# Optimization experiments

Measured on AMD Instinct MI355X. Metric: run time of the kernel, lower is better.

Reference implementation:

```python
import jax, jax.numpy as jnp
import numpy as np
import math

D_MODEL = 1024
NUM_HEADS = 16
HEAD_DIM = D_MODEL // NUM_HEADS  # 64


def setup_inputs() -> dict:
    key = jax.random.key(0)
    ks = jax.random.split(key, 5)
    B, T = 4, 2048
    scale = 1.0 / math.sqrt(D_MODEL)
    return {
        "x": jax.random.normal(ks[0], (B, T, D_MODEL), dtype=jnp.float32),
        "wq": jax.random.normal(ks[1], (D_MODEL, D_MODEL), dtype=jnp.float32) * scale,
        "wk": jax.random.normal(ks[2], (D_MODEL, D_MODEL), dtype=jnp.float32) * scale,
        "wv": jax.random.normal(ks[3], (D_MODEL, D_MODEL), dtype=jnp.float32) * scale,
        "wo": jax.random.normal(ks[4], (D_MODEL, D_MODEL), dtype=jnp.float32) * scale,
    }


def reference(x, wq, wk, wv, wo):
    B, T, _ = x.shape
    H, Dk = NUM_HEADS, HEAD_DIM

    def split_heads(t):  # [B,T,D] -> [B,H,T,Dk]
        return t.reshape(B, T, H, Dk).transpose(0, 2, 1, 3)

    q = split_heads(x @ wq)
    k = split_heads(x @ wk)
    v = split_heads(x @ wv)

    # scaled QK^T: [B,H,T,T]
    scores = jnp.einsum("bhqd,bhkd->bhqk", q, k) / jnp.sqrt(jnp.float32(Dk))
    # causal mask: triu(ones, diag=0).T.bool() == lower-triangular incl. diagonal
    causal = jnp.tril(jnp.ones((T, T), dtype=bool))
    scores = jnp.where(causal, scores, -jnp.inf)
    attn = jax.nn.softmax(scores, axis=-1)

    out = jnp.einsum("bhqk,bhkd->bhqd", attn, v)  # [B,H,T,Dk]
    out = out.transpose(0, 2, 1, 3).reshape(B, T, H * Dk)
    return out @ wo
```

## Files before the change

kernel.cpp:

```cpp
#include <hip/hip_runtime.h>
#include <hip/hip_bf16.h>
#include <stdint.h>

typedef __attribute__((ext_vector_type(8))) short bf16x8;
typedef __attribute__((ext_vector_type(4))) float f32x4;
typedef __attribute__((ext_vector_type(4))) unsigned short u16x4;
typedef __attribute__((ext_vector_type(4))) float float4v;

#define MFMA16(a, b, c) __builtin_amdgcn_mfma_f32_16x16x32_bf16((a), (b), (c), 0, 0, 0)

__device__ __forceinline__ unsigned short f2bf(float f) {
  return __builtin_bit_cast(unsigned short, (__bf16)f);
}

typedef const __attribute__((address_space(1))) void* gptr1_t;
typedef __attribute__((address_space(3))) void* lptr3_t;
__device__ __forceinline__ void gload16(const void* g, void* l) {
  __builtin_amdgcn_global_load_lds((gptr1_t)g, (lptr3_t)l, 16, 0, 0);
}

__global__ __launch_bounds__(256) void cvt_x_kernel(const float* __restrict__ in,
                                                    unsigned short* __restrict__ out) {
  int i = blockIdx.x * 256 + threadIdx.x;
  float4v f = ((const float4v*)in)[i];
  u16x4 o;
  o[0] = f2bf(f[0]); o[1] = f2bf(f[1]); o[2] = f2bf(f[2]); o[3] = f2bf(f[3]);
  ((u16x4*)out)[i] = o;
}

__global__ __launch_bounds__(256) void wt_cvt_kernel(const float* __restrict__ w0,
                                                     const float* __restrict__ w1,
                                                     const float* __restrict__ w2,
                                                     const float* __restrict__ w3,
                                                     unsigned short* __restrict__ out) {
  const float* in = blockIdx.z == 0 ? w0 : blockIdx.z == 1 ? w1 : blockIdx.z == 2 ? w2 : w3;
  unsigned short* o = out + (size_t)blockIdx.z * 1024 * 1024;
  __shared__ float tile[32][33];
  int tx = threadIdx.x & 31, ty = threadIdx.x >> 5;
  int c0 = blockIdx.x * 32, r0 = blockIdx.y * 32;
#pragma unroll
  for (int i = 0; i < 4; i++)
    tile[ty + 8 * i][tx] = in[(size_t)(r0 + ty + 8 * i) * 1024 + c0 + tx];
  __syncthreads();
#pragma unroll
  for (int i = 0; i < 4; i++)
    o[(size_t)(c0 + ty + 8 * i) * 1024 + r0 + tx] = f2bf(tile[tx][ty + 8 * i]);
}

template <bool OUTF32>
__global__ __launch_bounds__(256) void gemm128_kernel(
    const unsigned short* __restrict__ A,
    const unsigned short* __restrict__ B0, const unsigned short* __restrict__ B1,
    const unsigned short* __restrict__ B2,
    void* C0, void* C1, void* C2) {
  constexpr int K = 1024, N = 1024;
  const unsigned short* Bt = blockIdx.z == 0 ? B0 : blockIdx.z == 1 ? B1 : B2;
  void* Cv = blockIdx.z == 0 ? C0 : blockIdx.z == 1 ? C1 : C2;

  __shared__ unsigned short As[128 * 32];
  __shared__ unsigned short Bs[128 * 32];

  const int tid = threadIdx.x;
  const int w = tid >> 6, lane = tid & 63, l15 = lane & 15, l4 = lane >> 4;
  const int wm = w >> 1, wn = w & 1;
  const int m0 = blockIdx.x * 128, n0 = blockIdx.y * 128;

  f32x4 acc[4][4] = {};

  const int srow = w * 32 + (lane >> 2);
  const int scol = (lane & 3) * 8;
  const unsigned short* ga = A + (size_t)(m0 + srow) * K + scol;
  const unsigned short* gb = Bt + (size_t)(n0 + srow) * K + scol;
  char* lA = (char*)As + w * 2048;
  char* lB = (char*)Bs + w * 2048;

  for (int k0 = 0; k0 < K; k0 += 32) {
    __syncthreads();
    gload16(ga + k0, lA);
    gload16(ga + k0 + 16 * K, lA + 1024);
    gload16(gb + k0, lB);
    gload16(gb + k0 + 16 * K, lB + 1024);
    __syncthreads();

    bf16x8 af[4], bfr[4];
#pragma unroll
    for (int mi = 0; mi < 4; mi++)
      af[mi] = *(const bf16x8*)&As[(wm * 64 + mi * 16 + l15) * 32 + 8 * l4];
#pragma unroll
    for (int ni = 0; ni < 4; ni++)
      bfr[ni] = *(const bf16x8*)&Bs[(wn * 64 + ni * 16 + l15) * 32 + 8 * l4];
#pragma unroll
    for (int mi = 0; mi < 4; mi++)
#pragma unroll
      for (int ni = 0; ni < 4; ni++)
        acc[mi][ni] = MFMA16(af[mi], bfr[ni], acc[mi][ni]);
  }

#pragma unroll
  for (int mi = 0; mi < 4; mi++)
#pragma unroll
    for (int ni = 0; ni < 4; ni++)
#pragma unroll
      for (int r = 0; r < 4; r++) {
        int mg = m0 + wm * 64 + mi * 16 + 4 * l4 + r;
        int ng = n0 + wn * 64 + ni * 16 + l15;
        if (OUTF32)
          ((float*)Cv)[(size_t)mg * N + ng] = acc[mi][ni][r];
        else
          ((unsigned short*)Cv)[(size_t)mg * N + ng] = f2bf(acc[mi][ni][r]);
      }
}

__global__ __launch_bounds__(256) void gemm64_kernel(const unsigned short* __restrict__ A,
                                                     const unsigned short* __restrict__ Bt,
                                                     float* __restrict__ Cv) {
  constexpr int K = 1024, N = 1024;
  __shared__ unsigned short As[64 * 32];
  __shared__ unsigned short Bs[128 * 32];

  const int tid = threadIdx.x;
  const int w = tid >> 6, lane = tid & 63, l15 = lane & 15, l4 = lane >> 4;
  const int wm = w >> 1, wn = w & 1;
  const int m0 = blockIdx.x * 64, n0 = blockIdx.y * 128;

  f32x4 acc[2][4] = {};

  const int arow = w * 16 + (lane >> 2);
  const int brow = w * 32 + (lane >> 2);
  const int scol = (lane & 3) * 8;
  const unsigned short* ga = A + (size_t)(m0 + arow) * K + scol;
  const unsigned short* gb = Bt + (size_t)(n0 + brow) * K + scol;
  char* lA = (char*)As + w * 1024;
  char* lB = (char*)Bs + w * 2048;

  for (int k0 = 0; k0 < K; k0 += 32) {
    __syncthreads();
    gload16(ga + k0, lA);
    gload16(gb + k0, lB);
    gload16(gb + k0 + 16 * K, lB + 1024);
    __syncthreads();

    bf16x8 af[2], bfr[4];
#pragma unroll
    for (int mi = 0; mi < 2; mi++)
      af[mi] = *(const bf16x8*)&As[(wm * 32 + mi * 16 + l15) * 32 + 8 * l4];
#pragma unroll
    for (int ni = 0; ni < 4; ni++)
      bfr[ni] = *(const bf16x8*)&Bs[(wn * 64 + ni * 16 + l15) * 32 + 8 * l4];
#pragma unroll
    for (int mi = 0; mi < 2; mi++)
#pragma unroll
      for (int ni = 0; ni < 4; ni++)
        acc[mi][ni] = MFMA16(af[mi], bfr[ni], acc[mi][ni]);
  }

#pragma unroll
  for (int mi = 0; mi < 2; mi++)
#pragma unroll
    for (int ni = 0; ni < 4; ni++)
#pragma unroll
      for (int r = 0; r < 4; r++) {
        int mg = m0 + wm * 32 + mi * 16 + 4 * l4 + r;
        int ng = n0 + wn * 64 + ni * 16 + l15;
        Cv[(size_t)mg * N + ng] = acc[mi][ni][r];
      }
}

__global__ __launch_bounds__(256, 4) void attn_kernel(const unsigned short* __restrict__ Qb,
                                                      const unsigned short* __restrict__ Kb,
                                                      const unsigned short* __restrict__ Vb,
                                                      unsigned short* __restrict__ Ob) {
  const int bid = blockIdx.x;
  const int xcd = bid & 7, slot = bid >> 3;
  const int hb = xcd * 8 + (slot >> 4);
  const int p = slot & 15;
  const int h = hb & 15, bb = hb >> 4;

  const int tid = threadIdx.x, w = tid >> 6, lane = tid & 63, l15 = lane & 15, l4 = lane >> 4;

  __shared__ unsigned short K_lds[2][64 * 64];
  __shared__ unsigned short Vt_lds[2][64 * 64];
  __shared__ unsigned short P_lds[4][16 * 64];

  const size_t brow = (size_t)bb * 2048;
  const int qq = w * 16 + l15;
  const int sw = 8 * (l15 & 7);
  constexpr float C = 0.18033688f;

  const int qbA = p, qbB = 31 - p;
  const int lastB = qbB;

  bf16x8 qfA0, qfA1, qfB0, qfB1;
  {
    const unsigned short* qa = Qb + (brow + qbA * 64 + qq) * 1024 + h * 64 + 8 * l4;
    qfA0 = *(const bf16x8*)qa;
    qfA1 = *(const bf16x8*)(qa + 32);
    const unsigned short* qbp = Qb + (brow + qbB * 64 + qq) * 1024 + h * 64 + 8 * l4;
    qfB0 = *(const bf16x8*)qbp;
    qfB1 = *(const bf16x8*)(qbp + 32);
  }

  f32x4 oA[4] = {}, oB[4] = {};
  float mrA = -__builtin_inff(), lrA = 0.0f;
  float mrB = -__builtin_inff(), lrB = 0.0f;

  const int kcol = 8 * ((lane & 7) ^ ((lane >> 3) & 7));
  const unsigned short* gk = Kb + (brow + 8 * w + (lane >> 3)) * 1024 + h * 64 + kcol;
  const int vr0 = 2 * (tid >> 3);
  const int vsc = (tid & 7) * 8;
  const unsigned short* gv = Vb + (brow + vr0) * 1024 + h * 64 + vsc;

  auto vt_write = [&](int buf, const bf16x8& v0, const bf16x8& v1) {
#pragma unroll
    for (int j = 0; j < 8; j++) {
      const int d = vsc + j;
      const int msk = 8 * ((d ^ (d >> 3)) & 7);
      uint32_t pk = (uint32_t)(unsigned short)v0[j] |
                    ((uint32_t)(unsigned short)v1[j] << 16);
      *(uint32_t*)&Vt_lds[buf][d * 64 + (vr0 ^ msk)] = pk;
    }
  };

  auto tile_compute = [&](const unsigned short* Kc, const unsigned short* Vtc,
                          const bf16x8& q0f, const bf16x8& q1f, f32x4* oacc,
                          float& m_run, float& l_run, bool diag) {
    f32x4 s[4];
    __builtin_amdgcn_s_setprio(1);
#pragma unroll
    for (int sub = 0; sub < 4; ++sub) {
      const unsigned short* kr0 = &Kc[(sub * 16 + l15) * 64 + ((8 * l4) ^ sw)];
      const unsigned short* kr1 = &Kc[(sub * 16 + l15) * 64 + ((32 + 8 * l4) ^ sw)];
      f32x4 z = {0.f, 0.f, 0.f, 0.f};
      z = MFMA16(*(const bf16x8*)kr0, q0f, z);
      z = MFMA16(*(const bf16x8*)kr1, q1f, z);
      s[sub] = z;
    }
    __builtin_amdgcn_s_setprio(0);

    float mt = -__builtin_inff();
    if (diag) {
#pragma unroll
      for (int sub = 0; sub < 4; ++sub)
#pragma unroll
        for (int r4 = 0; r4 < 4; r4++) {
          const int kv_t = sub * 16 + 4 * l4 + r4;
          float sv = s[sub][r4];
          sv = (kv_t > qq) ? -__builtin_inff() : sv;
          s[sub][r4] = sv;
          mt = fmaxf(mt, sv);
        }
    } else {
#pragma unroll
      for (int sub = 0; sub < 4; ++sub)
#pragma unroll
        for (int r4 = 0; r4 < 4; r4++) mt = fmaxf(mt, s[sub][r4]);
    }
    mt = fmaxf(mt, __shfl_xor(mt, 16));
    mt = fmaxf(mt, __shfl_xor(mt, 32));

    float m_new = m_run;
    if (!__all(mt <= m_run + 44.3614f)) {
      m_new = fmaxf(m_run, mt);
      const float alpha = __builtin_amdgcn_exp2f((m_run - m_new) * C);
      const float ao0 = __shfl(alpha, 4 * l4 + 0);
      const float ao1 = __shfl(alpha, 4 * l4 + 1);
      const float ao2 = __shfl(alpha, 4 * l4 + 2);
      const float ao3 = __shfl(alpha, 4 * l4 + 3);
#pragma unroll
      for (int d = 0; d < 4; ++d) {
        oacc[d][0] *= ao0; oacc[d][1] *= ao1; oacc[d][2] *= ao2; oacc[d][3] *= ao3;
      }
      l_run *= alpha;
      m_run = m_new;
    }
    const float mnc = m_new * C;

    float lt = 0.0f;
#pragma unroll
    for (int sub = 0; sub < 4; ++sub) {
      u16x4 pw;
#pragma unroll
      for (int r4 = 0; r4 < 4; r4++) {
        float pv = __builtin_amdgcn_exp2f(__builtin_fmaf(s[sub][r4], C, -mnc));
        lt += pv;
        pw[r4] = f2bf(pv);
      }
      *(u16x4*)&P_lds[w][l15 * 64 + ((sub * 16 + 4 * l4) ^ sw)] = pw;
    }

    const bf16x8 pf0 = *(const bf16x8*)&P_lds[w][l15 * 64 + ((8 * l4) ^ sw)];
    const bf16x8 pf1 = *(const bf16x8*)&P_lds[w][l15 * 64 + ((32 + 8 * l4) ^ sw)];
    __builtin_amdgcn_s_setprio(1);
#pragma unroll
    for (int d = 0; d < 4; ++d) {
      const int dd = d * 16 + l15;
      const int vm = 8 * ((dd ^ (dd >> 3)) & 7);
      const unsigned short* vp0 = &Vtc[dd * 64 + ((8 * l4) ^ vm)];
      const unsigned short* vp1 = &Vtc[dd * 64 + ((32 + 8 * l4) ^ vm)];
      oacc[d] = MFMA16(pf0, *(const bf16x8*)vp0, oacc[d]);
      oacc[d] = MFMA16(pf1, *(const bf16x8*)vp1, oacc[d]);
    }
    __builtin_amdgcn_s_setprio(0);

    lt += __shfl_xor(lt, 16);
    lt += __shfl_xor(lt, 32);
    l_run += lt;
  };

  gload16(gk, (char*)K_lds[0] + w * 1024);
  gload16(gk + 32 * 1024, (char*)K_lds[0] + w * 1024 + 4096);
  {
    bf16x8 v0 = *(const bf16x8*)gv;
    bf16x8 v1 = *(const bf16x8*)(gv + 1024);
    vt_write(0, v0, v1);
  }
  __syncthreads();

  for (int kb = 0; kb <= lastB; ++kb) {
    const int cur = kb & 1, nxt = cur ^ 1;
    const bool pre = kb < lastB;
    bf16x8 pv0, pv1;
    if (pre) {
      const size_t off = (size_t)(kb + 1) * 64 * 1024;
      gload16(gk + off, (char*)K_lds[nxt] + w * 1024);
      gload16(gk + off + 32 * 1024, (char*)K_lds[nxt] + w * 1024 + 4096);
      pv0 = *(const bf16x8*)(gv + off);
      pv1 = *(const bf16x8*)(gv + off + 1024);
    }

    if (kb <= qbA)
      tile_compute(K_lds[cur], Vt_lds[cur], qfA0, qfA1, oA, mrA, lrA, kb == qbA);
    tile_compute(K_lds[cur], Vt_lds[cur], qfB0, qfB1, oB, mrB, lrB, kb == lastB);

    if (pre) vt_write(nxt, pv0, pv1);
    __syncthreads();
  }

  {
    const float linv = 1.0f / lrA;
    const float li[4] = {__shfl(linv, 4 * l4 + 0), __shfl(linv, 4 * l4 + 1),
                         __shfl(linv, 4 * l4 + 2), __shfl(linv, 4 * l4 + 3)};
#pragma unroll
    for (int d = 0; d < 4; ++d)
#pragma unroll
      for (int r4 = 0; r4 < 4; r4++) {
        const size_t orow = brow + qbA * 64 + w * 16 + 4 * l4 + r4;
        Ob[orow * 1024 + h * 64 + d * 16 + l15] = f2bf(oA[d][r4] * li[r4]);
      }
  }
  {
    const float linv = 1.0f / lrB;
    const float li[4] = {__shfl(linv, 4 * l4 + 0), __shfl(linv, 4 * l4 + 1),
                         __shfl(linv, 4 * l4 + 2), __shfl(linv, 4 * l4 + 3)};
#pragma unroll
    for (int d = 0; d < 4; ++d)
#pragma unroll
      for (int r4 = 0; r4 < 4; r4++) {
        const size_t orow = brow + qbB * 64 + w * 16 + 4 * l4 + r4;
        Ob[orow * 1024 + h * 64 + d * 16 + l15] = f2bf(oB[d][r4] * li[r4]);
      }
  }
}

extern "C" void kernel_launch(void* const* d_in, const int* in_sizes, int n_in,
                              void* d_out, int out_size, void* d_ws, size_t ws_size,
                              hipStream_t stream) {
  const float* x  = (const float*)d_in[0];
  const float* wq = (const float*)d_in[1];
  const float* wk = (const float*)d_in[2];
  const float* wv = (const float*)d_in[3];
  const float* wo = (const float*)d_in[4];

  char* ws = (char*)d_ws;
  unsigned short* Xb  = (unsigned short*)(ws);
  unsigned short* Wt  = (unsigned short*)(ws + (16u << 20));
  unsigned short* Wqt = Wt;
  unsigned short* Wkt = Wt + (1u << 20);
  unsigned short* Wvt = Wt + (2u << 20);
  unsigned short* Wot = Wt + (3u << 20);
  unsigned short* Qb  = (unsigned short*)(ws + (24u << 20));
  unsigned short* Kb  = (unsigned short*)(ws + (40u << 20));
  unsigned short* Vb  = (unsigned short*)(ws + (56u << 20));
  unsigned short* Ob  = Xb;

  cvt_x_kernel<<<8192, 256, 0, stream>>>(x, Xb);
  wt_cvt_kernel<<<dim3(32, 32, 4), 256, 0, stream>>>(wq, wk, wv, wo, Wt);
  gemm128_kernel<false><<<dim3(64, 8, 3), 256, 0, stream>>>(Xb, Wqt, Wkt, Wvt, Qb, Kb, Vb);
  attn_kernel<<<1024, 256, 0, stream>>>(Qb, Kb, Vb, Ob);
  gemm64_kernel<<<dim3(128, 8), 256, 0, stream>>>(Ob, Wot, (float*)d_out);
}
```

Baseline: 175.0 us.

## Double GEMM K-step, interleave two query tiles in attention, MFMA row sums

Both GEMM kernels now stage a 64-wide K slice per iteration instead of 32, which halves the number of barrier pairs per tile at the cost of twice the LDS. The attention loop is split into stages so that the QK products, softmax and PV products of the two query tiles interleave, giving the scheduler independent work to overlap MFMA with exp and LDS traffic. Row sums are now computed by an MFMA against a vector of bf16 ones instead of scalar adds and cross-lane shuffles, and the max reduction uses three-input max. This adds register pressure and sums the bf16-rounded probabilities rather than the fp32 ones.

```diff
diff --git a/kernel.cpp b/kernel.cpp
--- a/kernel.cpp
+++ b/kernel.cpp
@@ -11,6 +11,9 @@
 
 __device__ __forceinline__ unsigned short f2bf(float f) {
   return __builtin_bit_cast(unsigned short, (__bf16)f);
+}
+__device__ __forceinline__ float m3(float a, float b, float c) {
+  return fmaxf(fmaxf(a, b), c);
 }
 
 typedef const __attribute__((address_space(1))) void* gptr1_t;
@@ -57,8 +60,8 @@
   const unsigned short* Bt = blockIdx.z == 0 ? B0 : blockIdx.z == 1 ? B1 : B2;
   void* Cv = blockIdx.z == 0 ? C0 : blockIdx.z == 1 ? C1 : C2;
 
-  __shared__ unsigned short As[128 * 32];
-  __shared__ unsigned short Bs[128 * 32];
+  __shared__ unsigned short As[128 * 64];
+  __shared__ unsigned short Bs[128 * 64];
 
   const int tid = threadIdx.x;
   const int w = tid >> 6, lane = tid & 63, l15 = lane & 15, l4 = lane >> 4;
@@ -67,33 +70,37 @@
 
   f32x4 acc[4][4] = {};
 
-  const int srow = w * 32 + (lane >> 2);
-  const int scol = (lane & 3) * 8;
+  const int srow = w * 32 + (lane >> 3);
+  const int scol = (lane & 7) * 8;
   const unsigned short* ga = A + (size_t)(m0 + srow) * K + scol;
   const unsigned short* gb = Bt + (size_t)(n0 + srow) * K + scol;
-  char* lA = (char*)As + w * 2048;
-  char* lB = (char*)Bs + w * 2048;
-
-  for (int k0 = 0; k0 < K; k0 += 32) {
+  char* lA = (char*)As + w * 4096;
+  char* lB = (char*)Bs + w * 4096;
+
+  for (int k0 = 0; k0 < K; k0 += 64) {
     __syncthreads();
-    gload16(ga + k0, lA);
-    gload16(ga + k0 + 16 * K, lA + 1024);
-    gload16(gb + k0, lB);
-    gload16(gb + k0 + 16 * K, lB + 1024);
+#pragma unroll
+    for (int i = 0; i < 4; i++) {
+      gload16(ga + k0 + 8 * i * K, lA + i * 1024);
+      gload16(gb + k0 + 8 * i * K, lB + i * 1024);
+    }
     __syncthreads();
 
-    bf16x8 af[4], bfr[4];
-#pragma unroll
-    for (int mi = 0; mi < 4; mi++)
-      af[mi] = *(const bf16x8*)&As[(wm * 64 + mi * 16 + l15) * 32 + 8 * l4];
-#pragma unroll
-    for (int ni = 0; ni < 4; ni++)
-      bfr[ni] = *(const bf16x8*)&Bs[(wn * 64 + ni * 16 + l15) * 32 + 8 * l4];
-#pragma unroll
-    for (int mi = 0; mi < 4; mi++)
+#pragma unroll
+    for (int kk = 0; kk < 2; kk++) {
+      bf16x8 af[4], bfr[4];
+#pragma unroll
+      for (int mi = 0; mi < 4; mi++)
+        af[mi] = *(const bf16x8*)&As[(wm * 64 + mi * 16 + l15) * 64 + kk * 32 + 8 * l4];
 #pragma unroll
       for (int ni = 0; ni < 4; ni++)
-        acc[mi][ni] = MFMA16(af[mi], bfr[ni], acc[mi][ni]);
+        bfr[ni] = *(const bf16x8*)&Bs[(wn * 64 + ni * 16 + l15) * 64 + kk * 32 + 8 * l4];
+#pragma unroll
+      for (int mi = 0; mi < 4; mi++)
+#pragma unroll
+        for (int ni = 0; ni < 4; ni++)
+          acc[mi][ni] = MFMA16(af[mi], bfr[ni], acc[mi][ni]);
+    }
   }
 
 #pragma unroll
@@ -115,8 +122,8 @@
                                                      const unsigned short* __restrict__ Bt,
                                                      float* __restrict__ Cv) {
   constexpr int K = 1024, N = 1024;
-  __shared__ unsigned short As[64 * 32];
-  __shared__ unsigned short Bs[128 * 32];
+  __shared__ unsigned short As[64 * 64];
+  __shared__ unsigned short Bs[128 * 64];
 
   const int tid = threadIdx.x;
   const int w = tid >> 6, lane = tid & 63, l15 = lane & 15, l4 = lane >> 4;
@@ -125,33 +132,39 @@
 
   f32x4 acc[2][4] = {};
 
-  const int arow = w * 16 + (lane >> 2);
-  const int brow = w * 32 + (lane >> 2);
-  const int scol = (lane & 3) * 8;
+  const int arow = w * 16 + (lane >> 3);
+  const int brow = w * 32 + (lane >> 3);
+  const int scol = (lane & 7) * 8;
   const unsigned short* ga = A + (size_t)(m0 + arow) * K + scol;
   const unsigned short* gb = Bt + (size_t)(n0 + brow) * K + scol;
-  char* lA = (char*)As + w * 1024;
-  char* lB = (char*)Bs + w * 2048;
-
-  for (int k0 = 0; k0 < K; k0 += 32) {
+  char* lA = (char*)As + w * 2048;
+  char* lB = (char*)Bs + w * 4096;
+
+  for (int k0 = 0; k0 < K; k0 += 64) {
     __syncthreads();
-    gload16(ga + k0, lA);
-    gload16(gb + k0, lB);
-    gload16(gb + k0 + 16 * K, lB + 1024);
+#pragma unroll
+    for (int i = 0; i < 2; i++)
+      gload16(ga + k0 + 8 * i * K, lA + i * 1024);
+#pragma unroll
+    for (int i = 0; i < 4; i++)
+      gload16(gb + k0 + 8 * i * K, lB + i * 1024);
     __syncthreads();
 
-    bf16x8 af[2], bfr[4];
-#pragma unroll
-    for (int mi = 0; mi < 2; mi++)
-      af[mi] = *(const bf16x8*)&As[(wm * 32 + mi * 16 + l15) * 32 + 8 * l4];
-#pragma unroll
-    for (int ni = 0; ni < 4; ni++)
-      bfr[ni] = *(const bf16x8*)&Bs[(wn * 64 + ni * 16 + l15) * 32 + 8 * l4];
-#pragma unroll
-    for (int mi = 0; mi < 2; mi++)
+#pragma unroll
+    for (int kk = 0; kk < 2; kk++) {
+      bf16x8 af[2], bfr[4];
+#pragma unroll
+      for (int mi = 0; mi < 2; mi++)
+        af[mi] = *(const bf16x8*)&As[(wm * 32 + mi * 16 + l15) * 64 + kk * 32 + 8 * l4];
 #pragma unroll
       for (int ni = 0; ni < 4; ni++)
-        acc[mi][ni] = MFMA16(af[mi], bfr[ni], acc[mi][ni]);
+        bfr[ni] = *(const bf16x8*)&Bs[(wn * 64 + ni * 16 + l15) * 64 + kk * 32 + 8 * l4];
+#pragma unroll
+      for (int mi = 0; mi < 2; mi++)
+#pragma unroll
+        for (int ni = 0; ni < 4; ni++)
+          acc[mi][ni] = MFMA16(af[mi], bfr[ni], acc[mi][ni]);
+    }
   }
 
 #pragma unroll
@@ -186,6 +199,7 @@
   const int qq = w * 16 + l15;
   const int sw = 8 * (l15 & 7);
   constexpr float C = 0.18033688f;
+  const bf16x8 ones = {0x3F80, 0x3F80, 0x3F80, 0x3F80, 0x3F80, 0x3F80, 0x3F80, 0x3F80};
 
   const int qbA = p, qbB = 31 - p;
   const int lastB = qbB;
@@ -201,8 +215,8 @@
   }
 
   f32x4 oA[4] = {}, oB[4] = {};
-  float mrA = -__builtin_inff(), lrA = 0.0f;
-  float mrB = -__builtin_inff(), lrB = 0.0f;
+  f32x4 lA4 = {0.f, 0.f, 0.f, 0.f}, lB4 = {0.f, 0.f, 0.f, 0.f};
+  float mrA = -__builtin_inff(), mrB = -__builtin_inff();
 
   const int kcol = 8 * ((lane & 7) ^ ((lane >> 3) & 7));
   const unsigned short* gk = Kb + (brow + 8 * w + (lane >> 3)) * 1024 + h * 64 + kcol;
@@ -221,11 +235,7 @@
     }
   };
 
-  auto tile_compute = [&](const unsigned short* Kc, const unsigned short* Vtc,
-                          const bf16x8& q0f, const bf16x8& q1f, f32x4* oacc,
-                          float& m_run, float& l_run, bool diag) {
-    f32x4 s[4];
-    __builtin_amdgcn_s_setprio(1);
+  auto qk8 = [&](const unsigned short* Kc, const bf16x8& q0f, const bf16x8& q1f, f32x4* s) {
 #pragma unroll
     for (int sub = 0; sub < 4; ++sub) {
       const unsigned short* kr0 = &Kc[(sub * 16 + l15) * 64 + ((8 * l4) ^ sw)];
@@ -235,32 +245,28 @@
       z = MFMA16(*(const bf16x8*)kr1, q1f, z);
       s[sub] = z;
     }
-    __builtin_amdgcn_s_setprio(0);
-
-    float mt = -__builtin_inff();
+  };
+
+  auto maskmax = [&](f32x4* s, float& m_run, f32x4* oacc, f32x4& lacc, bool diag) {
     if (diag) {
 #pragma unroll
       for (int sub = 0; sub < 4; ++sub)
 #pragma unroll
         for (int r4 = 0; r4 < 4; r4++) {
           const int kv_t = sub * 16 + 4 * l4 + r4;
-          float sv = s[sub][r4];
-          sv = (kv_t > qq) ? -__builtin_inff() : sv;
-          s[sub][r4] = sv;
-          mt = fmaxf(mt, sv);
+          s[sub][r4] = (kv_t > qq) ? -__builtin_inff() : s[sub][r4];
         }
-    } else {
-#pragma unroll
-      for (int sub = 0; sub < 4; ++sub)
-#pragma unroll
-        for (int r4 = 0; r4 < 4; r4++) mt = fmaxf(mt, s[sub][r4]);
-    }
+    }
+    const float t0 = m3(s[0][0], s[0][1], s[0][2]);
+    const float t1 = m3(s[0][3], s[1][0], s[1][1]);
+    const float t2 = m3(s[1][2], s[1][3], s[2][0]);
+    const float t3 = m3(s[2][1], s[2][2], s[2][3]);
+    const float t4 = m3(s[3][0], s[3][1], s[3][2]);
+    float mt = fmaxf(m3(t0, t1, t2), m3(t3, t4, s[3][3]));
     mt = fmaxf(mt, __shfl_xor(mt, 16));
     mt = fmaxf(mt, __shfl_xor(mt, 32));
-
-    float m_new = m_run;
     if (!__all(mt <= m_run + 44.3614f)) {
-      m_new = fmaxf(m_run, mt);
+      const float m_new = fmaxf(m_run, mt);
       const float alpha = __builtin_amdgcn_exp2f((m_run - m_new) * C);
       const float ao0 = __shfl(alpha, 4 * l4 + 0);
       const float ao1 = __shfl(alpha, 4 * l4 + 1);
@@ -270,41 +276,41 @@
       for (int d = 0; d < 4; ++d) {
         oacc[d][0] *= ao0; oacc[d][1] *= ao1; oacc[d][2] *= ao2; oacc[d][3] *= ao3;
       }
-      l_run *= alpha;
+      lacc[0] *= ao0; lacc[1] *= ao1; lacc[2] *= ao2; lacc[3] *= ao3;
       m_run = m_new;
     }
-    const float mnc = m_new * C;
-
-    float lt = 0.0f;
-#pragma unroll
-    for (int sub = 0; sub < 4; ++sub) {
-      u16x4 pw;
-#pragma unroll
-      for (int r4 = 0; r4 < 4; r4++) {
-        float pv = __builtin_amdgcn_exp2f(__builtin_fmaf(s[sub][r4], C, -mnc));
-        lt += pv;
-        pw[r4] = f2bf(pv);
-      }
-      *(u16x4*)&P_lds[w][l15 * 64 + ((sub * 16 + 4 * l4) ^ sw)] = pw;
-    }
-
-    const bf16x8 pf0 = *(const bf16x8*)&P_lds[w][l15 * 64 + ((8 * l4) ^ sw)];
-    const bf16x8 pf1 = *(const bf16x8*)&P_lds[w][l15 * 64 + ((32 + 8 * l4) ^ sw)];
-    __builtin_amdgcn_s_setprio(1);
+  };
+
+  auto expcvt = [&](const f32x4* s, float m_run, u16x4* pw) {
+    const float mnc = m_run * C;
+#pragma unroll
+    for (int sub = 0; sub < 4; ++sub)
+#pragma unroll
+      for (int r4 = 0; r4 < 4; r4++)
+        pw[sub][r4] = f2bf(__builtin_amdgcn_exp2f(__builtin_fmaf(s[sub][r4], C, -mnc)));
+  };
+
+  auto pstore = [&](const u16x4* pw) {
+#pragma unroll
+    for (int sub = 0; sub < 4; ++sub)
+      *(u16x4*)&P_lds[w][l15 * 64 + ((sub * 16 + 4 * l4) ^ sw)] = pw[sub];
+  };
+
+  auto pload = [&](bf16x8& p0, bf16x8& p1) {
+    p0 = *(const bf16x8*)&P_lds[w][l15 * 64 + ((8 * l4) ^ sw)];
+    p1 = *(const bf16x8*)&P_lds[w][l15 * 64 + ((32 + 8 * l4) ^ sw)];
+  };
+
+  auto pv8 = [&](const unsigned short* Vtc, const bf16x8& p0, const bf16x8& p1, f32x4* oacc) {
 #pragma unroll
     for (int d = 0; d < 4; ++d) {
       const int dd = d * 16 + l15;
       const int vm = 8 * ((dd ^ (dd >> 3)) & 7);
       const unsigned short* vp0 = &Vtc[dd * 64 + ((8 * l4) ^ vm)];
       const unsigned short* vp1 = &Vtc[dd * 64 + ((32 + 8 * l4) ^ vm)];
-      oacc[d] = MFMA16(pf0, *(const bf16x8*)vp0, oacc[d]);
-      oacc[d] = MFMA16(pf1, *(const bf16x8*)vp1, oacc[d]);
-    }
-    __builtin_amdgcn_s_setprio(0);
-
-    lt += __shfl_xor(lt, 16);
-    lt += __shfl_xor(lt, 32);
-    l_run += lt;
+      oacc[d] = MFMA16(p0, *(const bf16x8*)vp0, oacc[d]);
+      oacc[d] = MFMA16(p1, *(const bf16x8*)vp1, oacc[d]);
+    }
   };
 
   gload16(gk, (char*)K_lds[0] + w * 1024);
@@ -319,6 +325,8 @@
   for (int kb = 0; kb <= lastB; ++kb) {
     const int cur = kb & 1, nxt = cur ^ 1;
     const bool pre = kb < lastB;
+    const unsigned short* Kc = K_lds[cur];
+    const unsigned short* Vtc = Vt_lds[cur];
     bf16x8 pv0, pv1;
     if (pre) {
       const size_t off = (size_t)(kb + 1) * 64 * 1024;
@@ -328,18 +336,59 @@
       pv1 = *(const bf16x8*)(gv + off + 1024);
     }
 
-    if (kb <= qbA)
-      tile_compute(K_lds[cur], Vt_lds[cur], qfA0, qfA1, oA, mrA, lrA, kb == qbA);
-    tile_compute(K_lds[cur], Vt_lds[cur], qfB0, qfB1, oB, mrB, lrB, kb == lastB);
+    if (kb <= qbA) {
+      f32x4 sA[4], sB[4];
+      __builtin_amdgcn_s_setprio(1);
+      qk8(Kc, qfA0, qfA1, sA);
+      qk8(Kc, qfB0, qfB1, sB);
+      __builtin_amdgcn_s_setprio(0);
+
+      u16x4 pwA[4], pwB[4];
+      maskmax(sA, mrA, oA, lA4, kb == qbA);
+      expcvt(sA, mrA, pwA);
+      pstore(pwA);
+      maskmax(sB, mrB, oB, lB4, false);
+      expcvt(sB, mrB, pwB);
+
+      bf16x8 pA0, pA1;
+      pload(pA0, pA1);
+      __builtin_amdgcn_s_setprio(1);
+      pv8(Vtc, pA0, pA1, oA);
+      __builtin_amdgcn_s_setprio(0);
+      pstore(pwB);
+      lA4 = MFMA16(pA0, ones, lA4);
+      lA4 = MFMA16(pA1, ones, lA4);
+      bf16x8 pB0, pB1;
+      pload(pB0, pB1);
+      __builtin_amdgcn_s_setprio(1);
+      pv8(Vtc, pB0, pB1, oB);
+      lB4 = MFMA16(pB0, ones, lB4);
+      lB4 = MFMA16(pB1, ones, lB4);
+      __builtin_amdgcn_s_setprio(0);
+    } else {
+      f32x4 sB[4];
+      __builtin_amdgcn_s_setprio(1);
+      qk8(Kc, qfB0, qfB1, sB);
+      __builtin_amdgcn_s_setprio(0);
+      u16x4 pwB[4];
+      maskmax(sB, mrB, oB, lB4, kb == lastB);
+      expcvt(sB, mrB, pwB);
+      pstore(pwB);
+      bf16x8 pB0, pB1;
+      pload(pB0, pB1);
+      __builtin_amdgcn_s_setprio(1);
+      pv8(Vtc, pB0, pB1, oB);
+      lB4 = MFMA16(pB0, ones, lB4);
+      lB4 = MFMA16(pB1, ones, lB4);
+      __builtin_amdgcn_s_setprio(0);
+    }
 
     if (pre) vt_write(nxt, pv0, pv1);
     __syncthreads();
   }
 
   {
-    const float linv = 1.0f / lrA;
-    const float li[4] = {__shfl(linv, 4 * l4 + 0), __shfl(linv, 4 * l4 + 1),
-                         __shfl(linv, 4 * l4 + 2), __shfl(linv, 4 * l4 + 3)};
+    const float li[4] = {1.0f / lA4[0], 1.0f / lA4[1], 1.0f / lA4[2], 1.0f / lA4[3]};
 #pragma unroll
     for (int d = 0; d < 4; ++d)
 #pragma unroll
@@ -349,9 +398,7 @@
       }
   }
   {
-    const float linv = 1.0f / lrB;
-    const float li[4] = {__shfl(linv, 4 * l4 + 0), __shfl(linv, 4 * l4 + 1),
-                         __shfl(linv, 4 * l4 + 2), __shfl(linv, 4 * l4 + 3)};
+    const float li[4] = {1.0f / lB4[0], 1.0f / lB4[1], 1.0f / lB4[2], 1.0f / lB4[3]};
 #pragma unroll
     for (int d = 0; d < 4; ++d)
 #pragma unroll
```

Measured after the change: 445.7 us. 155% more time.
